# Optimization experiments

Measured on AMD Instinct MI355X. Metric: run time of the kernel, lower is better.

## Reference

```python
import jax, jax.numpy as jnp
import numpy as np

B, S, DIN, DOUT = 4, 2048, 4096, 4096
QMAX = 127  # 2**(8-1) - 1


def setup_inputs() -> dict:
    key = jax.random.key(0)
    k_x, k_w, k_b, k_ws = jax.random.split(key, 4)
    x = jax.random.normal(k_x, (B, S, DIN), dtype=jnp.float32)
    # int8-valued weights stored as int32 (as in the torch module's .int() weight)
    weight = jax.random.randint(k_w, (DOUT, DIN), -QMAX, QMAX + 1, dtype=jnp.int32)
    bias = jax.random.randint(k_b, (DOUT,), -10, 11, dtype=jnp.int32)
    # per-input-channel weight scale, shape (out_features, 1)
    weight_scale = (jax.random.uniform(k_ws, (DOUT, 1), dtype=jnp.float32) * 0.01 + 1e-4)
    input_scale = jnp.float32(0.02)
    output_scale = jnp.float32(0.05)
    return {
        "x": x,
        "weight": weight,
        "bias": bias,
        "weight_scale": weight_scale,
        "input_scale": input_scale,
        "output_scale": output_scale,
    }


def reference(x, weight, bias, weight_scale, input_scale, output_scale):
    # fake-quantize activations: round to int grid, then dequantize back to float
    xq = jnp.round(x / input_scale).astype(jnp.int32).astype(jnp.float32) * input_scale
    # dequantize weights: (O, I)
    w = weight.astype(jnp.float32) * weight_scale
    # fp32 GEMM: [B,S,I] x [I,O] -> [B,S,O]
    ret = jnp.einsum("bsi,oi->bso", xq, w)
    ret = ret + bias.astype(jnp.float32)
    # requantize output to int grid (int32 output, as in torch .int())
    return jnp.round(ret / output_scale).astype(jnp.int32)
```

## Files before the change

### kernel.cpp

```cpp
#include <hip/hip_runtime.h>
#include <stdint.h>

#define MDIM 8192
#define KDIM 4096
#define NDIM 4096

typedef float f32x4 __attribute__((ext_vector_type(4)));
typedef __bf16 bf16x8 __attribute__((ext_vector_type(8)));
typedef short short8 __attribute__((ext_vector_type(8)));
typedef float fl4 __attribute__((ext_vector_type(4)));
typedef int i32x4 __attribute__((ext_vector_type(4)));

__device__ __forceinline__ short f2bf_bits(float f) {
    unsigned int u = __float_as_uint(f);
    u += 0x7fffu + ((u >> 16) & 1u);
    return (short)(u >> 16);
}

__device__ __forceinline__ void gload_lds16(const void* g, void* l) {
    __builtin_amdgcn_global_load_lds(
        (__attribute__((address_space(1))) void*)(uintptr_t)g,
        (__attribute__((address_space(3))) void*)(uintptr_t)l,
        16, 0, 0);
}

__global__ void __launch_bounds__(256) quant_x_kernel(const float* __restrict__ x,
                                                      short* __restrict__ xq,
                                                      const float* __restrict__ p_is) {
    const float inv_is = 1.0f / p_is[0];
    const int64_t i = ((int64_t)blockIdx.x * 256 + threadIdx.x) * 8;
    fl4 a = *(const fl4*)(x + i);
    fl4 b = *(const fl4*)(x + i + 4);
    short8 o;
    o[0] = f2bf_bits(rintf(a[0] * inv_is));
    o[1] = f2bf_bits(rintf(a[1] * inv_is));
    o[2] = f2bf_bits(rintf(a[2] * inv_is));
    o[3] = f2bf_bits(rintf(a[3] * inv_is));
    o[4] = f2bf_bits(rintf(b[0] * inv_is));
    o[5] = f2bf_bits(rintf(b[1] * inv_is));
    o[6] = f2bf_bits(rintf(b[2] * inv_is));
    o[7] = f2bf_bits(rintf(b[3] * inv_is));
    *(short8*)(xq + i) = o;
}

__global__ void __launch_bounds__(256) quant_w_kernel(const int* __restrict__ w,
                                                      short* __restrict__ wq) {
    const int64_t i = ((int64_t)blockIdx.x * 256 + threadIdx.x) * 8;
    i32x4 a = *(const i32x4*)(w + i);
    i32x4 b = *(const i32x4*)(w + i + 4);
    short8 o;
    o[0] = f2bf_bits((float)a[0]);
    o[1] = f2bf_bits((float)a[1]);
    o[2] = f2bf_bits((float)a[2]);
    o[3] = f2bf_bits((float)a[3]);
    o[4] = f2bf_bits((float)b[0]);
    o[5] = f2bf_bits((float)b[1]);
    o[6] = f2bf_bits((float)b[2]);
    o[7] = f2bf_bits((float)b[3]);
    *(short8*)(wq + i) = o;
}

__global__ void __launch_bounds__(256) gemm_bf16_kernel(
    const short* __restrict__ A,
    const short* __restrict__ Bw,
    const int* __restrict__ bias,
    const float* __restrict__ wscale,
    const float* __restrict__ p_is,
    const float* __restrict__ p_os,
    int* __restrict__ out) {
    __shared__ __align__(16) short As[128 * 32];
    __shared__ __align__(16) short Bs[128 * 32];

    const int tid  = threadIdx.x;
    const int lane = tid & 63;
    const int wave = tid >> 6;
    const int quad = lane >> 4;
    const int r16  = lane & 15;
    const int rsw  = (r16 >> 1) & 3;

    const int n0 = blockIdx.x * 128;
    const int m0 = blockIdx.y * 128;

    const int wm = (wave & 1) * 64;
    const int wn = (wave >> 1) * 64;

    const int srow   = tid >> 2;
    const int schunk = (tid & 3) ^ ((srow >> 1) & 3);
    const short* gA0 = A  + (int64_t)(m0 + srow) * KDIM + schunk * 8;
    const short* gB0 = Bw + (int64_t)(n0 + srow) * KDIM + schunk * 8;

    short* lA0 = As + wave * 512;
    short* lA1 = As + 2048 + wave * 512;
    short* lB0 = Bs + wave * 512;
    short* lB1 = Bs + 2048 + wave * 512;

    f32x4 acc[4][4];
#pragma unroll
    for (int i = 0; i < 4; ++i)
#pragma unroll
        for (int j = 0; j < 4; ++j) acc[i][j] = (f32x4)0.0f;

    for (int k0 = 0; k0 < KDIM; k0 += 32) {
        __syncthreads();
        gload_lds16(gA0 + k0, lA0);
        gload_lds16(gA0 + k0 + 64 * KDIM, lA1);
        gload_lds16(gB0 + k0, lB0);
        gload_lds16(gB0 + k0 + 64 * KDIM, lB1);
        __syncthreads();

        bf16x8 af[4], bfr[4];
#pragma unroll
        for (int mi = 0; mi < 4; ++mi)
            af[mi] = *(const bf16x8*)(As + (wm + mi * 16 + r16) * 32 + (quad ^ rsw) * 8);
#pragma unroll
        for (int ni = 0; ni < 4; ++ni)
            bfr[ni] = *(const bf16x8*)(Bs + (wn + ni * 16 + r16) * 32 + (quad ^ rsw) * 8);

#pragma unroll
        for (int mi = 0; mi < 4; ++mi)
#pragma unroll
            for (int ni = 0; ni < 4; ++ni)
                acc[mi][ni] = __builtin_amdgcn_mfma_f32_16x16x32_bf16(
                    af[mi], bfr[ni], acc[mi][ni], 0, 0, 0);
    }

    const float is = p_is[0];
    const float inv_os = 1.0f / p_os[0];

    float alpha[4], beta[4];
#pragma unroll
    for (int ni = 0; ni < 4; ++ni) {
        const int col = n0 + wn + ni * 16 + r16;
        alpha[ni] = is * wscale[col] * inv_os;
        beta[ni]  = (float)bias[col] * inv_os;
    }

#pragma unroll
    for (int mi = 0; mi < 4; ++mi) {
        const int row0 = m0 + wm + mi * 16 + quad * 4;
#pragma unroll
        for (int ni = 0; ni < 4; ++ni) {
            const int col = n0 + wn + ni * 16 + r16;
#pragma unroll
            for (int reg = 0; reg < 4; ++reg) {
                const float v = acc[mi][ni][reg] * alpha[ni] + beta[ni];
                out[(int64_t)(row0 + reg) * NDIM + col] = __float2int_rn(v);
            }
        }
    }
}

extern "C" void kernel_launch(void* const* d_in, const int* in_sizes, int n_in,
                              void* d_out, int out_size, void* d_ws, size_t ws_size,
                              hipStream_t stream) {
    (void)in_sizes; (void)n_in; (void)out_size; (void)ws_size;
    const float* x      = (const float*)d_in[0];
    const int*   weight = (const int*)d_in[1];
    const int*   bias   = (const int*)d_in[2];
    const float* wscale = (const float*)d_in[3];
    const float* p_is   = (const float*)d_in[4];
    const float* p_os   = (const float*)d_in[5];

    short* xq = (short*)d_ws;
    short* wq = xq + (size_t)MDIM * KDIM;

    quant_x_kernel<<<(int)(((int64_t)MDIM * KDIM) / 2048), 256, 0, stream>>>(x, xq, p_is);
    quant_w_kernel<<<(int)(((int64_t)NDIM * KDIM) / 2048), 256, 0, stream>>>(weight, wq);

    dim3 grid(NDIM / 128, MDIM / 128);
    gemm_bf16_kernel<<<grid, 256, 0, stream>>>(xq, wq, bias, wscale, p_is, p_os, (int*)d_out);
}
```

Before: 559.9 us.

## Fuse activation and weight quantization into GEMM tile loads with register prefetch

Drops the two standalone bf16 conversion kernels and has the GEMM read fp32 activations and int32 weights directly. Each tile is converted to bf16 in registers and written to LDS, and the next tile is prefetched into registers while the MFMAs run. This removes the workspace round trip and two launches. The cost is that every GEMM block re-reads and re-converts 4-byte source data, doubling tile-load traffic, and the async global-to-LDS loads are replaced by register staging, which adds register pressure.

```diff
diff --git a/kernel.cpp b/kernel.cpp
--- a/kernel.cpp
+++ b/kernel.cpp
@@ -17,20 +17,7 @@
     return (short)(u >> 16);
 }
 
-__device__ __forceinline__ void gload_lds16(const void* g, void* l) {
-    __builtin_amdgcn_global_load_lds(
-        (__attribute__((address_space(1))) void*)(uintptr_t)g,
-        (__attribute__((address_space(3))) void*)(uintptr_t)l,
-        16, 0, 0);
-}
-
-__global__ void __launch_bounds__(256) quant_x_kernel(const float* __restrict__ x,
-                                                      short* __restrict__ xq,
-                                                      const float* __restrict__ p_is) {
-    const float inv_is = 1.0f / p_is[0];
-    const int64_t i = ((int64_t)blockIdx.x * 256 + threadIdx.x) * 8;
-    fl4 a = *(const fl4*)(x + i);
-    fl4 b = *(const fl4*)(x + i + 4);
+__device__ __forceinline__ short8 cvt_x8(fl4 a, fl4 b, float inv_is) {
     short8 o;
     o[0] = f2bf_bits(rintf(a[0] * inv_is));
     o[1] = f2bf_bits(rintf(a[1] * inv_is));
@@ -40,14 +27,10 @@
     o[5] = f2bf_bits(rintf(b[1] * inv_is));
     o[6] = f2bf_bits(rintf(b[2] * inv_is));
     o[7] = f2bf_bits(rintf(b[3] * inv_is));
-    *(short8*)(xq + i) = o;
+    return o;
 }
 
-__global__ void __launch_bounds__(256) quant_w_kernel(const int* __restrict__ w,
-                                                      short* __restrict__ wq) {
-    const int64_t i = ((int64_t)blockIdx.x * 256 + threadIdx.x) * 8;
-    i32x4 a = *(const i32x4*)(w + i);
-    i32x4 b = *(const i32x4*)(w + i + 4);
+__device__ __forceinline__ short8 cvt_w8(i32x4 a, i32x4 b) {
     short8 o;
     o[0] = f2bf_bits((float)a[0]);
     o[1] = f2bf_bits((float)a[1]);
@@ -57,12 +40,12 @@
     o[5] = f2bf_bits((float)b[1]);
     o[6] = f2bf_bits((float)b[2]);
     o[7] = f2bf_bits((float)b[3]);
-    *(short8*)(wq + i) = o;
+    return o;
 }
 
-__global__ void __launch_bounds__(256) gemm_bf16_kernel(
-    const short* __restrict__ A,
-    const short* __restrict__ Bw,
+__global__ void __launch_bounds__(256) gemm_fused_kernel(
+    const float* __restrict__ x,
+    const int* __restrict__ w,
     const int* __restrict__ bias,
     const float* __restrict__ wscale,
     const float* __restrict__ p_is,
@@ -84,15 +67,21 @@
     const int wm = (wave & 1) * 64;
     const int wn = (wave >> 1) * 64;
 
+    const float inv_is = 1.0f / p_is[0];
+
     const int srow   = tid >> 2;
-    const int schunk = (tid & 3) ^ ((srow >> 1) & 3);
-    const short* gA0 = A  + (int64_t)(m0 + srow) * KDIM + schunk * 8;
-    const short* gB0 = Bw + (int64_t)(n0 + srow) * KDIM + schunk * 8;
+    const int chunk  = tid & 3;
+    const int pchunk = chunk ^ ((srow >> 1) & 3);
 
-    short* lA0 = As + wave * 512;
-    short* lA1 = As + 2048 + wave * 512;
-    short* lB0 = Bs + wave * 512;
-    short* lB1 = Bs + 2048 + wave * 512;
+    const float* gA  = x + (int64_t)(m0 + srow) * KDIM + chunk * 8;
+    const float* gA2 = gA + (int64_t)64 * KDIM;
+    const int*   gB  = w + (int64_t)(n0 + srow) * KDIM + chunk * 8;
+    const int*   gB2 = gB + (int64_t)64 * KDIM;
+
+    short* wA0 = As + srow * 32 + pchunk * 8;
+    short* wA1 = As + (srow + 64) * 32 + pchunk * 8;
+    short* wB0 = Bs + srow * 32 + pchunk * 8;
+    short* wB1 = Bs + (srow + 64) * 32 + pchunk * 8;
 
     f32x4 acc[4][4];
 #pragma unroll
@@ -100,12 +89,36 @@
 #pragma unroll
         for (int j = 0; j < 4; ++j) acc[i][j] = (f32x4)0.0f;
 
+    fl4   ar0, ar1, ar2, ar3;
+    i32x4 br0, br1, br2, br3;
+#define LOAD_TILE(k)                                    \
+    do {                                                \
+        ar0 = *(const fl4*)(gA + (k));                  \
+        ar1 = *(const fl4*)(gA + (k) + 4);              \
+        ar2 = *(const fl4*)(gA2 + (k));                 \
+        ar3 = *(const fl4*)(gA2 + (k) + 4);             \
+        br0 = *(const i32x4*)(gB + (k));                \
+        br1 = *(const i32x4*)(gB + (k) + 4);            \
+        br2 = *(const i32x4*)(gB2 + (k));               \
+        br3 = *(const i32x4*)(gB2 + (k) + 4);           \
+    } while (0)
+
+    LOAD_TILE(0);
+
     for (int k0 = 0; k0 < KDIM; k0 += 32) {
+        short8 sa0 = cvt_x8(ar0, ar1, inv_is);
+        short8 sa1 = cvt_x8(ar2, ar3, inv_is);
+        short8 sb0 = cvt_w8(br0, br1);
+        short8 sb1 = cvt_w8(br2, br3);
+
         __syncthreads();
-        gload_lds16(gA0 + k0, lA0);
-        gload_lds16(gA0 + k0 + 64 * KDIM, lA1);
-        gload_lds16(gB0 + k0, lB0);
-        gload_lds16(gB0 + k0 + 64 * KDIM, lB1);
+        *(short8*)wA0 = sa0;
+        *(short8*)wA1 = sa1;
+        *(short8*)wB0 = sb0;
+        *(short8*)wB1 = sb1;
+
+        if (k0 + 32 < KDIM) LOAD_TILE(k0 + 32);
+
         __syncthreads();
 
         bf16x8 af[4], bfr[4];
@@ -123,6 +136,7 @@
                 acc[mi][ni] = __builtin_amdgcn_mfma_f32_16x16x32_bf16(
                     af[mi], bfr[ni], acc[mi][ni], 0, 0, 0);
     }
+#undef LOAD_TILE
 
     const float is = p_is[0];
     const float inv_os = 1.0f / p_os[0];
@@ -153,7 +167,7 @@
 extern "C" void kernel_launch(void* const* d_in, const int* in_sizes, int n_in,
                               void* d_out, int out_size, void* d_ws, size_t ws_size,
                               hipStream_t stream) {
-    (void)in_sizes; (void)n_in; (void)out_size; (void)ws_size;
+    (void)in_sizes; (void)n_in; (void)out_size; (void)d_ws; (void)ws_size;
     const float* x      = (const float*)d_in[0];
     const int*   weight = (const int*)d_in[1];
     const int*   bias   = (const int*)d_in[2];
@@ -161,12 +175,7 @@
     const float* p_is   = (const float*)d_in[4];
     const float* p_os   = (const float*)d_in[5];
 
-    short* xq = (short*)d_ws;
-    short* wq = xq + (size_t)MDIM * KDIM;
-
-    quant_x_kernel<<<(int)(((int64_t)MDIM * KDIM) / 2048), 256, 0, stream>>>(x, xq, p_is);
-    quant_w_kernel<<<(int)(((int64_t)NDIM * KDIM) / 2048), 256, 0, stream>>>(weight, wq);
-
     dim3 grid(NDIM / 128, MDIM / 128);
-    gemm_bf16_kernel<<<grid, 256, 0, stream>>>(xq, wq, bias, wscale, p_is, p_os, (int*)d_out);
+    gemm_fused_kernel<<<grid, 256, 0, stream>>>(x, weight, bias, wscale, p_is, p_os,
+                                                (int*)d_out);
 }
```

Measured after the change: 762.2 us. 1.36x slower.
